# Kernel tuning notes

Measured on AMD Instinct MI355X. Metric: run time of the kernel, lower is better.

## Reference

```python
import jax, jax.numpy as jnp
import numpy as np
from jax import lax

V = 9; C1 = 80; C2 = 40; C4 = 24; CH = 32
H1, W1 = 30, 40; H2, W2 = 60, 80; H4, W4 = 120, 160
SHAPE = (96, 96, 96); N = 131072; EPS = 1e-5
OFFS = np.stack(np.meshgrid(np.arange(-1, 2), np.arange(-1, 2), np.arange(-1, 2), indexing='ij'), -1).reshape(-1, 3).astype(np.int32)  # 27 kernel offsets


def conv2d(x, w, b):
    y = lax.conv_general_dilated(x, w, (1, 1), 'SAME', dimension_numbers=('NCHW', 'OIHW', 'NCHW'))
    return y + b[None, :, None, None]


def bn1d(x, g, b):  # eval-mode BatchNorm1d (running_mean=0, running_var=1)
    return g * x * (1.0 / np.sqrt(1.0 + EPS)) + b


def layernorm(x, g, b):
    m = x.mean(-1, keepdims=True)
    v = ((x - m) ** 2).mean(-1, keepdims=True)
    return (x - m) / jnp.sqrt(v + EPS) * g + b


def grid_sample_zeros(img, gx, gy):
    # img [V,C,H,W]; gx,gy [V,M] normalized to [-1,1]; bilinear, align_corners=True, zeros padding
    Vn, C, H, W = img.shape
    px = (gx + 1.0) * 0.5 * (W - 1)
    py = (gy + 1.0) * 0.5 * (H - 1)
    x0 = jnp.floor(px); y0 = jnp.floor(py)
    wx = px - x0; wy = py - y0
    flat = img.reshape(Vn, C, H * W)
    def corner(xc, yc, wgt):
        valid = (xc >= 0) & (xc <= W - 1) & (yc >= 0) & (yc <= H - 1)
        xi = jnp.clip(xc, 0, W - 1).astype(jnp.int32)
        yi = jnp.clip(yc, 0, H - 1).astype(jnp.int32)
        idx = yi * W + xi  # [V,M]
        g = jax.vmap(lambda f, i: f[:, i])(flat, idx)  # [V,C,M]
        return g * (wgt * valid)[:, None, :]
    return (corner(x0, y0, (1 - wx) * (1 - wy)) + corner(x0 + 1, y0, wx * (1 - wy))
            + corner(x0, y0 + 1, (1 - wx) * wy) + corner(x0 + 1, y0 + 1, wx * wy))


def subm_conv(feat, W3, cxyz, grid):
    # submanifold sparse 3x3x3 conv: per-offset gather of active neighbors -> GEMM -> accumulate
    n = feat.shape[0]
    shp = jnp.asarray(SHAPE, jnp.int32)
    out = jnp.zeros((n, W3.shape[-1]), feat.dtype)
    for k in range(27):
        nc = cxyz + jnp.asarray(OFFS[k])
        inb = jnp.all((nc >= 0) & (nc < shp), axis=1)
        ncc = jnp.clip(nc, 0, shp - 1)
        idx = grid[ncc[:, 0], ncc[:, 1], ncc[:, 2]]
        ok = (inb & (idx >= 0)).astype(feat.dtype)
        g = feat[jnp.clip(idx, 0, n - 1)] * ok[:, None]
        out = out + g @ W3[k]
    return out


def _forward(feats_1x, feats_2x, feats_4x, origin, voxel_size, KRcam,
             w_f1, b_f1, w_f2, b_f2, w_f4, b_f4, w_down, b_down,
             w_p1, b_p1, w_p2, b_p2, w_p3, b_p3, w_p4, b_p4,
             bn0_g, bn0_b, w_elan, w_s1, ln1_g, ln1_b, w_s2, ln2_g, ln2_b,
             w_s3, ln3_g, ln3_b, w_s4, bn4_g, bn4_b,
             coords, stage, min_view_number):
    # feat_fusion_pre (bs=1, take batch 0)
    f1 = jax.nn.relu(conv2d(feats_1x[:, 0], w_f1, b_f1))
    f2 = jax.nn.relu(conv2d(feats_2x[:, 0], w_f2, b_f2))
    f4 = jax.nn.relu(conv2d(feats_4x[:, 0], w_f4, b_f4))
    f1 = jax.image.resize(f1, (V, C1, H2, W2), 'bilinear')  # F.interpolate x2
    f4 = f4.reshape(V, C4, H2, 2, W2, 2).mean(axis=(3, 5))  # AvgPool2d(2)
    fuse = jnp.concatenate([f1, f2, f4], axis=1)
    fuse = jax.nn.relu(conv2d(fuse, w_down, b_down))
    for w, b in ((w_p1, b_p1), (w_p2, b_p2), (w_p3, b_p3), (w_p4, b_p4)):
        fuse = fuse + jax.nn.relu(conv2d(fuse, w, b))  # residual blocks -> [V,CH,H2,W2]
    # multi-view projection
    cxyz = coords[:, 1:]
    world = cxyz.astype(jnp.float32) * voxel_size + origin[0]
    hom = jnp.concatenate([world, jnp.ones_like(world[:, :1])], axis=1)  # [N,4]
    im_p = jnp.einsum('vij,nj->vin', KRcam[:, 0], hom)  # [V,3,N]
    im_z = im_p[:, 2]
    gx = 2.0 * (im_p[:, 0] / im_z) / (W4 - 1) - 1.0
    gy = 2.0 * (im_p[:, 1] / im_z) / (H4 - 1) - 1.0
    mask = (jnp.abs(gx) <= 1) & (jnp.abs(gy) <= 1) & (im_z > 0)  # [V,N]
    count = mask.sum(0).astype(jnp.float32)
    # inputs are constructed so every voxel is seen by all views: valid_voxel compaction == identity
    feats = grid_sample_zeros(fuse, gx, gy) * mask[:, None, :]  # [V,CH,N]
    feat = feats.transpose(2, 0, 1)  # [N,V,CH]
    m = mask.T.astype(feat.dtype)  # [N,V]
    den = m.sum(1, keepdims=True)
    mean = (m[..., None] * feat).sum(1) / den
    var = (m[..., None] * (feat - mean[:, None, :]) ** 2).sum(1) / den  # [N,CH]
    # sparse subm conv chain
    sc = cxyz // (2 ** (2 - stage))  # stage=2 -> identity
    grid = jnp.full(SHAPE, -1, jnp.int32).at[sc[:, 0], sc[:, 1], sc[:, 2]].set(jnp.arange(N, dtype=jnp.int32))
    x = bn1d(var, bn0_g, bn0_b)
    x = jax.nn.relu(subm_conv(x, w_elan, sc, grid))  # Spares3dELAN stand-in
    r = jax.nn.relu(subm_conv(x, w_s1, sc, grid)); x = layernorm(r + x, ln1_g, ln1_b)
    r = jax.nn.relu(subm_conv(x, w_s2, sc, grid)); x = layernorm(r + x, ln2_g, ln2_b)
    r = jax.nn.relu(subm_conv(x, w_s3, sc, grid)); x = layernorm(r + x, ln3_g, ln3_b)
    occ = bn1d(subm_conv(x, w_s4, sc, grid), bn4_g, bn4_b)  # [N,1]
    return occ, coords, count


def setup_inputs() -> dict:
    key = jax.random.key(0)
    keys = jax.random.split(key, 40)
    ki = iter(range(40))
    def rn(shape, s=1.0):
        return jax.random.normal(keys[next(ki)], shape, jnp.float32) * s
    inp = {}
    inp['feats_1x'] = rn((V, 1, C1, H1, W1))
    inp['feats_2x'] = rn((V, 1, C2, H2, W2))
    inp['feats_4x'] = rn((V, 1, C4, H4, W4))
    flat = np.arange(N, dtype=np.int64) * 6  # unique active voxels in a 96^3 grid
    cx = flat // (96 * 96); rem = flat % (96 * 96)
    inp['coords'] = jnp.asarray(np.stack([np.zeros(N, np.int64), cx, rem // 96, rem % 96], 1), jnp.int32)
    inp['origin'] = jnp.asarray([[-1.92, -1.92, 1.0]], jnp.float32)
    inp['voxel_size'] = jnp.float32(0.04)
    fx, fy = 38.0, 28.0
    P = np.zeros((V, 1, 3, 4), np.float32)
    for v in range(V):
        P[v, 0] = np.array([[fx, 0.0, (W4 - 1) / 2, fx * 0.02 * (v - 4)],
                            [0.0, fy, (H4 - 1) / 2, 0.0],
                            [0.0, 0.0, 1.0, 0.0]], np.float32)
    inp['KRcam'] = jnp.asarray(P)
    s = 0.05
    inp['w_f1'] = rn((C1, C1, 3, 3), s); inp['b_f1'] = rn((C1,), s)
    inp['w_f2'] = rn((C2, C2, 3, 3), s); inp['b_f2'] = rn((C2,), s)
    inp['w_f4'] = rn((C4, C4, 3, 3), s); inp['b_f4'] = rn((C4,), s)
    inp['w_down'] = rn((CH, C1 + C2 + C4, 1, 1), s); inp['b_down'] = rn((CH,), s)
    for i in (1, 2, 3, 4):
        inp['w_p%d' % i] = rn((CH, CH, 3, 3), s); inp['b_p%d' % i] = rn((CH,), s)
    inp['bn0_g'] = jnp.ones((CH,), jnp.float32); inp['bn0_b'] = jnp.zeros((CH,), jnp.float32)
    inp['w_elan'] = rn((27, CH, CH), s)
    inp['w_s1'] = rn((27, CH, CH), s); inp['ln1_g'] = jnp.ones((CH,), jnp.float32); inp['ln1_b'] = jnp.zeros((CH,), jnp.float32)
    inp['w_s2'] = rn((27, CH, CH), s); inp['ln2_g'] = jnp.ones((CH,), jnp.float32); inp['ln2_b'] = jnp.zeros((CH,), jnp.float32)
    inp['w_s3'] = rn((27, CH, CH), s); inp['ln3_g'] = jnp.ones((CH,), jnp.float32); inp['ln3_b'] = jnp.zeros((CH,), jnp.float32)
    inp['w_s4'] = rn((27, CH, 1), s); inp['bn4_g'] = jnp.ones((1,), jnp.float32); inp['bn4_b'] = jnp.zeros((1,), jnp.float32)
    inp['stage'] = 2
    inp['min_view_number'] = 1
    return inp


def reference(feats_1x, feats_2x, feats_4x, origin, voxel_size, KRcam,
              w_f1, b_f1, w_f2, b_f2, w_f4, b_f4, w_down, b_down,
              w_p1, b_p1, w_p2, b_p2, w_p3, b_p3, w_p4, b_p4,
              bn0_g, bn0_b, w_elan, w_s1, ln1_g, ln1_b, w_s2, ln2_g, ln2_b,
              w_s3, ln3_g, ln3_b, w_s4, bn4_g, bn4_b,
              coords, stage, min_view_number):
    return _forward(feats_1x, feats_2x, feats_4x, origin, voxel_size, KRcam,
                    w_f1, b_f1, w_f2, b_f2, w_f4, b_f4, w_down, b_down,
                    w_p1, b_p1, w_p2, b_p2, w_p3, b_p3, w_p4, b_p4,
                    bn0_g, bn0_b, w_elan, w_s1, ln1_g, ln1_b, w_s2, ln2_g, ln2_b,
                    w_s3, ln3_g, ln3_b, w_s4, bn4_g, bn4_b,
                    coords, stage, min_view_number)
```

## Files before the change

kernel.cpp:

```cpp
#include <hip/hip_runtime.h>
#include <math.h>

#define VN 9
#define NVOX 131072
#define GS 96
static constexpr float INVS = 0.9999950000374997f;

typedef short bf16x8 __attribute__((ext_vector_type(8)));
typedef float f32x4v __attribute__((ext_vector_type(4)));

__device__ inline float4 ld4(const float* p){ return *reinterpret_cast<const float4*>(p); }

__device__ inline ushort f2b(float f){
  unsigned u = __float_as_uint(f);
  unsigned r = (u + 0x7fffu + ((u >> 16) & 1u)) >> 16;
  return (ushort)r;
}
__device__ inline float b2f(ushort s){ return __uint_as_float(((unsigned)s) << 16); }
__device__ inline float blo(unsigned u){ return __uint_as_float(u << 16); }
__device__ inline float bhi(unsigned u){ return __uint_as_float(u & 0xffff0000u); }

__device__ inline float4 ld4b(const ushort* p){
  uint2 u = *reinterpret_cast<const uint2*>(p);
  float4 r; r.x = blo(u.x); r.y = bhi(u.x); r.z = blo(u.y); r.w = bhi(u.y); return r;
}
__device__ inline void st4b(ushort* p, float4 v){
  uint2 u;
  u.x = (unsigned)f2b(v.x) | ((unsigned)f2b(v.y) << 16);
  u.y = (unsigned)f2b(v.z) | ((unsigned)f2b(v.w) << 16);
  *reinterpret_cast<uint2*>(p) = u;
}

__device__ inline void wprep2_dev(const float* __restrict__ w, ushort* __restrict__ o,
                                  int Cout, int Cin, int K, int CK, int CoutPad, int tid){
  int ci32 = tid & 31;
  int co = (tid >> 5) % CoutPad;
  int ck = (tid / (32*CoutPad)) % CK;
  int tap = tid / (32*CoutPad*CK);
  int ci = ck*32 + ci32;
  float v = 0.f;
  if (co < Cout && ci < Cin) v = w[(size_t)(co*Cin + ci)*K*K + tap];
  o[tid] = f2b(v);
}
__device__ inline void wprep_dev(const float* __restrict__ w, ushort* __restrict__ o, int tid){
  int k = tid >> 10;
  int r = tid & 1023;
  int co = r >> 5;
  int ci = r & 31;
  o[tid] = f2b(w[k*1024 + ci*32 + co]);
}

__device__ inline void nhwc_tile_dev(const float* __restrict__ in, ushort* __restrict__ out,
                                     int C, int Cpad, int HW, int tile, int tilesPerV,
                                     float* lds, int tx){
  int v  = tile / tilesPerV;
  int p0 = (tile - v*tilesPerV) * 64;
  const float* ip = in + (size_t)v*C*HW + p0;
  int iters = Cpad >> 2;
  for (int i = 0; i < iters; ++i){
    int idx = i*256 + tx;
    int c = idx >> 6;
    int p = idx & 63;
    float val = 0.f;
    if (c < C && (p0 + p) < HW) val = ip[(size_t)c*HW + p];
    lds[c*65 + p] = val;
  }
  __syncthreads();
  int groups = Cpad >> 2;
  int tot = 64*groups;
  for (int basei = 0; basei < tot; basei += 256){
    int idx = basei + tx;
    if (idx < tot){
      int g  = idx % groups;
      int px = idx / groups;
      if ((p0 + px) < HW){
        float4 r;
        r.x = lds[(g*4+0)*65 + px];
        r.y = lds[(g*4+1)*65 + px];
        r.z = lds[(g*4+2)*65 + px];
        r.w = lds[(g*4+3)*65 + px];
        st4b(out + (size_t)(v*HW + p0 + px)*Cpad + g*4, r);
      }
    }
  }
}

__global__ __launch_bounds__(256) void k_prep(
    const float* wf1s, const float* wf2s, const float* wf4s, const float* wdns,
    const float* wp0s, const float* wp1s, const float* wp2s, const float* wp3s,
    const float* wes, const float* ws1s, const float* ws2s, const float* ws3s,
    ushort* wf1, ushort* wf2, ushort* wf4, ushort* wdn,
    ushort* wp0, ushort* wp1, ushort* wp2, ushort* wp3,
    ushort* w2e, ushort* w2s1, ushort* w2s2, ushort* w2s3,
    int* grid,
    const float* f1, const float* f2, const float* f4,
    ushort* o1, ushort* o2, ushort* o4){
  __shared__ float lds[96*65];
  int bid = blockIdx.x;
  int tx = threadIdx.x;
  if (bid < 270){ int t = bid*256+tx; if (t < 69120) wprep2_dev(wf1s, wf1, 80, 80, 3, 3, 80, t); return; }
  bid -= 270;
  if (bid < 108){ int t = bid*256+tx; if (t < 27648) wprep2_dev(wf2s, wf2, 40, 40, 3, 2, 48, t); return; }
  bid -= 108;
  if (bid < 36){ int t = bid*256+tx; if (t < 9216) wprep2_dev(wf4s, wf4, 24, 24, 3, 1, 32, t); return; }
  bid -= 36;
  if (bid < 20){ int t = bid*256+tx; if (t < 5120) wprep2_dev(wdns, wdn, 32, 144, 1, 5, 32, t); return; }
  bid -= 20;
  if (bid < 36){ int t = bid*256+tx; if (t < 9216) wprep2_dev(wp0s, wp0, 32, 32, 3, 1, 32, t); return; }
  bid -= 36;
  if (bid < 36){ int t = bid*256+tx; if (t < 9216) wprep2_dev(wp1s, wp1, 32, 32, 3, 1, 32, t); return; }
  bid -= 36;
  if (bid < 36){ int t = bid*256+tx; if (t < 9216) wprep2_dev(wp2s, wp2, 32, 32, 3, 1, 32, t); return; }
  bid -= 36;
  if (bid < 36){ int t = bid*256+tx; if (t < 9216) wprep2_dev(wp3s, wp3, 32, 32, 3, 1, 32, t); return; }
  bid -= 36;
  if (bid < 108){ int t = bid*256+tx; if (t < 27648) wprep_dev(wes, w2e, t); return; }
  bid -= 108;
  if (bid < 108){ int t = bid*256+tx; if (t < 27648) wprep_dev(ws1s, w2s1, t); return; }
  bid -= 108;
  if (bid < 108){ int t = bid*256+tx; if (t < 27648) wprep_dev(ws2s, w2s2, t); return; }
  bid -= 108;
  if (bid < 108){ int t = bid*256+tx; if (t < 27648) wprep_dev(ws3s, w2s3, t); return; }
  bid -= 108;
  if (bid < 3456){ int t = bid*256+tx; if (t < GS*GS*GS) grid[t] = -1; return; }
  bid -= 3456;
  if (bid < 171){ nhwc_tile_dev(f1, o1, 80, 96, 1200, bid, 19, lds, tx); return; }
  bid -= 171;
  if (bid < 675){ nhwc_tile_dev(f2, o2, 40, 64, 4800, bid, 75, lds, tx); return; }
  bid -= 675;
  if (bid < 2700){ nhwc_tile_dev(f4, o4, 24, 32, 19200, bid, 300, lds, tx); }
}

template<int CK, int NT, int TAPS, int MT>
__global__ __launch_bounds__(256) void k_conv_mfma(
    const ushort* __restrict__ fin, const ushort* __restrict__ w2,
    const float* __restrict__ bias, ushort* __restrict__ outp,
    int H, int W, int total, int Cout, int outStride, int outOff,
    const ushort* __restrict__ skipin){
  constexpr int CIN = CK*32;
  constexpr int COP = NT*16;
  int lane = threadIdx.x & 63;
  int wave = threadIdx.x >> 6;
  int vbase = blockIdx.x*(MT*64) + wave*(MT*16);
  int m = lane & 15, q = lane >> 4;
  int HW = H*W;
  int p[MT], py[MT], px[MT]; bool pin[MT];
  #pragma unroll
  for (int t = 0; t < MT; ++t){
    int pp = vbase + t*16 + m;
    pin[t] = pp < total;
    if (pp > total-1) pp = total-1;
    p[t] = pp;
    int v = pp / HW; int rem = pp - v*HW;
    int y = rem / W;
    py[t] = y; px[t] = rem - y*W;
  }
  f32x4v acc[MT][NT];
  #pragma unroll
  for (int t = 0; t < MT; ++t)
    #pragma unroll
    for (int n = 0; n < NT; ++n) acc[t][n] = 0.f;
  bf16x8 z = (short)0;

  #pragma unroll 1
  for (int tap = 0; tap < TAPS; ++tap){
    int dy = (TAPS == 9) ? tap/3 - 1 : 0;
    int dx = (TAPS == 9) ? tap%3 - 1 : 0;
    int off = dy*W + dx;
    bool val[MT];
    #pragma unroll
    for (int t = 0; t < MT; ++t)
      val[t] = pin[t] && ((unsigned)(py[t]+dy) < (unsigned)H)
                      && ((unsigned)(px[t]+dx) < (unsigned)W);
    #pragma unroll
    for (int ck = 0; ck < CK; ++ck){
      bf16x8 Af[MT], Bf[NT];
      #pragma unroll
      for (int t = 0; t < MT; ++t){
        size_t idx = val[t] ? (size_t)(p[t]+off) : 0;
        bf16x8 a = *(const bf16x8*)(fin + idx*CIN + ck*32 + q*8);
        Af[t] = val[t] ? a : z;
      }
      #pragma unroll
      for (int n = 0; n < NT; ++n)
        Bf[n] = *(const bf16x8*)(w2 + ((size_t)((tap*CK+ck)*COP + n*16 + m))*32 + q*8);
      #pragma unroll
      for (int t = 0; t < MT; ++t)
        #pragma unroll
        for (int n = 0; n < NT; ++n)
          acc[t][n] = __builtin_amdgcn_mfma_f32_16x16x32_bf16(Af[t], Bf[n], acc[t][n], 0, 0, 0);
    }
  }

  #pragma unroll
  for (int n = 0; n < NT; ++n){
    int co = n*16 + m;
    bool cok = co < Cout;
    float bs = cok ? bias[co] : 0.f;
    #pragma unroll
    for (int t = 0; t < MT; ++t){
      #pragma unroll
      for (int r = 0; r < 4; ++r){
        int pp = vbase + t*16 + q*4 + r;
        if (pp < total && cok){
          float x = fmaxf(acc[t][n][r] + bs, 0.f);
          if (skipin) x += b2f(skipin[(size_t)pp*CIN + co]);
          outp[(size_t)pp*outStride + outOff + co] = f2b(x);
        }
      }
    }
  }
}

__global__ void k_respool(const ushort* __restrict__ t1, const ushort* __restrict__ t4,
                          ushort* __restrict__ fc){
  int tid = blockIdx.x*256 + threadIdx.x;
  if (tid < 864000){
    int c4 = tid % 20;
    int x  = (tid / 20) % 80;
    int y  = (tid / 1600) % 60;
    int v  = tid / 96000;
    int c = c4*4;
    int ky = y >> 1; int y0, y1; float wy0, wy1;
    if ((y & 1) == 0){ y0 = ky-1; y1 = ky; wy0 = 0.25f; wy1 = 0.75f; if (y0 < 0){ y0 = 0; wy0 = 0.f; wy1 = 1.f; } }
    else             { y0 = ky; y1 = ky+1; wy0 = 0.75f; wy1 = 0.25f; if (y1 > 29){ y1 = 29; wy1 = 0.f; wy0 = 1.f; } }
    int kx = x >> 1; int x0, x1; float wx0, wx1;
    if ((x & 1) == 0){ x0 = kx-1; x1 = kx; wx0 = 0.25f; wx1 = 0.75f; if (x0 < 0){ x0 = 0; wx0 = 0.f; wx1 = 1.f; } }
    else             { x0 = kx; x1 = kx+1; wx0 = 0.75f; wx1 = 0.25f; if (x1 > 39){ x1 = 39; wx1 = 0.f; wx0 = 1.f; } }
    float4 a00 = ld4b(t1 + ((size_t)(v*30 + y0)*40 + x0)*80 + c);
    float4 a01 = ld4b(t1 + ((size_t)(v*30 + y0)*40 + x1)*80 + c);
    float4 a10 = ld4b(t1 + ((size_t)(v*30 + y1)*40 + x0)*80 + c);
    float4 a11 = ld4b(t1 + ((size_t)(v*30 + y1)*40 + x1)*80 + c);
    float w00 = wy0*wx0, w01 = wy0*wx1, w10 = wy1*wx0, w11 = wy1*wx1;
    float4 r;
    r.x = w00*a00.x + w01*a01.x + w10*a10.x + w11*a11.x;
    r.y = w00*a00.y + w01*a01.y + w10*a10.y + w11*a11.y;
    r.z = w00*a00.z + w01*a01.z + w10*a10.z + w11*a11.z;
    r.w = w00*a00.w + w01*a01.w + w10*a10.w + w11*a11.w;
    st4b(fc + ((size_t)(v*60 + y)*80 + x)*160 + c, r);
    return;
  }
  int t = tid - 864000;
  if (t >= 432000) return;
  int c4 = t % 10;
  int x  = (t / 10) % 80;
  int y  = (t / 800) % 60;
  int v  = t / 48000;
  if (c4 < 6){
    int c = c4*4;
    const ushort* b0 = t4 + ((size_t)(v*120 + 2*y)*160 + 2*x)*24 + c;
    float4 a = ld4b(b0), b = ld4b(b0 + 24), cc = ld4b(b0 + 160*24), d = ld4b(b0 + 160*24 + 24);
    float4 r;
    r.x = 0.25f*(a.x + b.x + cc.x + d.x);
    r.y = 0.25f*(a.y + b.y + cc.y + d.y);
    r.z = 0.25f*(a.z + b.z + cc.z + d.z);
    r.w = 0.25f*(a.w + b.w + cc.w + d.w);
    st4b(fc + ((size_t)(v*60 + y)*80 + x)*160 + 120 + c, r);
  } else {
    float4 zz = {0.f,0.f,0.f,0.f};
    st4b(fc + ((size_t)(v*60 + y)*80 + x)*160 + 144 + (c4-6)*4, zz);
  }
}

__global__ void k_scatter(const int* __restrict__ coords, const int* __restrict__ stage,
                          int* __restrict__ grid, int* __restrict__ scn,
                          float* __restrict__ coords_out,
                          const float* __restrict__ origin, const float* __restrict__ vsz,
                          const float* __restrict__ KR,
                          uint4* __restrict__ samp, float* __restrict__ cnt){
  int n = blockIdx.x*256 + threadIdx.x;
  if (n >= NVOX) return;
  int c0 = coords[n*4], c1 = coords[n*4+1], c2 = coords[n*4+2], c3 = coords[n*4+3];
  coords_out[n*4+0] = (float)c0;
  coords_out[n*4+1] = (float)c1;
  coords_out[n*4+2] = (float)c2;
  coords_out[n*4+3] = (float)c3;
  int sh = 2 - stage[0];
  int s1 = c1 >> sh, s2 = c2 >> sh, s3 = c3 >> sh;
  scn[n*3+0] = s1; scn[n*3+1] = s2; scn[n*3+2] = s3;
  grid[(s1*GS + s2)*GS + s3] = n;

  float vs = vsz[0];
  float wx = (float)c1*vs + origin[0];
  float wy = (float)c2*vs + origin[1];
  float wz = (float)c3*vs + origin[2];
  float den = 0.f;
  #pragma unroll 1
  for (int v = 0; v < VN; ++v){
    const float* P = KR + v*12;
    float ix = P[0]*wx + P[1]*wy + P[2]*wz + P[3];
    float iy = P[4]*wx + P[5]*wy + P[6]*wz + P[7];
    float iz = P[8]*wx + P[9]*wy + P[10]*wz + P[11];
    float rz = 1.f/iz;
    float gx = 2.f*(ix*rz)/159.f - 1.f;
    float gy = 2.f*(iy*rz)/119.f - 1.f;
    bool ok = (fabsf(gx) <= 1.f) && (fabsf(gy) <= 1.f) && (iz > 0.f);
    float px = ok ? (gx + 1.f)*0.5f*79.f : 0.f;
    float py = ok ? (gy + 1.f)*0.5f*59.f : 0.f;
    float x0f = floorf(px), y0f = floorf(py);
    float fx = px - x0f, fy = py - y0f;
    int idx = (int)y0f*80 + (int)x0f;
    float mf = ok ? 1.f : 0.f;
    float w00 = (1.f-fx)*(1.f-fy)*mf, w01 = fx*(1.f-fy)*mf;
    float w10 = (1.f-fx)*fy*mf,       w11 = fx*fy*mf;
    uint4 s;
    s.x = (unsigned)idx;
    s.y = (unsigned)f2b(w00) | ((unsigned)f2b(w01) << 16);
    s.z = (unsigned)f2b(w10) | ((unsigned)f2b(w11) << 16);
    s.w = 0;
    samp[(size_t)v*NVOX + n] = s;
    den += mf;
  }
  cnt[n] = den;
}

__global__ __launch_bounds__(256) void k_nbr_sample(
    const int* __restrict__ scn, const int* __restrict__ grid,
    int* __restrict__ nbr, unsigned* __restrict__ gmask16,
    const ushort* __restrict__ fuse, const uint4* __restrict__ samp,
    const float* __restrict__ cnt, const float* __restrict__ bn0g,
    const float* __restrict__ bn0b, ushort* __restrict__ F0){
  if (blockIdx.x < 512){
    int n = blockIdx.x*256 + threadIdx.x;
    int lane = threadIdx.x & 63;
    int sx = scn[n*3+0], sy = scn[n*3+1], sz = scn[n*3+2];
    unsigned msk = 0;
    #pragma unroll 1
    for (int k = 0; k < 27; ++k){
      int dx = k/9 - 1, dy = (k/3)%3 - 1, dz = k%3 - 1;
      int nx = sx+dx, ny = sy+dy, nz = sz+dz;
      int idx = -1;
      if (((unsigned)nx < 96u) && ((unsigned)ny < 96u) && ((unsigned)nz < 96u))
        idx = grid[(nx*GS + ny)*GS + nz];
      nbr[k*NVOX + n] = idx;
      unsigned long long b = __ballot(idx >= 0);
      unsigned sub = (unsigned)((b >> ((lane >> 4)*16)) & 0xFFFFull);
      if (sub) msk |= (1u << k);
    }
    if ((lane & 15) == 0) gmask16[n >> 4] = msk;
    return;
  }
  int tid = (blockIdx.x - 512)*256 + threadIdx.x;
  int vox = tid >> 3;
  int c4 = tid & 7;
  int c = c4*4;
  float s0=0.f,s1=0.f,s2=0.f,s3=0.f;
  float q0=0.f,q1=0.f,q2=0.f,q3=0.f;
  #pragma unroll 1
  for (int v = 0; v < VN; ++v){
    uint4 sv = samp[(size_t)v*NVOX + vox];
    float w00 = blo(sv.y), w01 = bhi(sv.y);
    float w10 = blo(sv.z), w11 = bhi(sv.z);
    const ushort* bp = fuse + (size_t)v*153600 + (size_t)sv.x*32 + c;
    float4 a00 = ld4b(bp);
    float4 a01 = ld4b(bp + 32);
    float4 a10 = ld4b(bp + 2560);
    float4 a11 = ld4b(bp + 2592);
    float g0 = w00*a00.x + w01*a01.x + w10*a10.x + w11*a11.x;
    float g1 = w00*a00.y + w01*a01.y + w10*a10.y + w11*a11.y;
    float g2 = w00*a00.z + w01*a01.z + w10*a10.z + w11*a11.z;
    float g3 = w00*a00.w + w01*a01.w + w10*a10.w + w11*a11.w;
    s0 += g0; q0 += g0*g0;
    s1 += g1; q1 += g1*g1;
    s2 += g2; q2 += g2*g2;
    s3 += g3; q3 += g3*g3;
  }
  float iden = 1.f/cnt[vox];
  float m0 = s0*iden, m1 = s1*iden, m2 = s2*iden, m3 = s3*iden;
  float4 g = ld4(bn0g + c);
  float4 b = ld4(bn0b + c);
  float4 r;
  r.x = g.x*fmaxf(q0*iden - m0*m0, 0.f)*INVS + b.x;
  r.y = g.y*fmaxf(q1*iden - m1*m1, 0.f)*INVS + b.y;
  r.z = g.z*fmaxf(q2*iden - m2*m2, 0.f)*INVS + b.z;
  r.w = g.w*fmaxf(q3*iden - m3*m3, 0.f)*INVS + b.w;
  st4b(F0 + (size_t)vox*32 + c, r);
}

template<int MODE>
__global__ __launch_bounds__(256, 8) void k_subm_mfma(
    const ushort* __restrict__ fin, const ushort* __restrict__ w2,
    const int* __restrict__ nbr, const unsigned* __restrict__ gmask16,
    const float* __restrict__ lng, const float* __restrict__ lnb,
    ushort* __restrict__ fout){
  int lane = threadIdx.x & 63;
  int wave = threadIdx.x >> 6;
  int vb = blockIdx.x*64 + wave*16;
  int m = lane & 15;
  int q = lane >> 4;

  f32x4v acc0 = 0.f, acc1 = 0.f;
  bf16x8 zc = (short)0;
  unsigned rem = gmask16[vb >> 4];
  int id = -1;
  int k = -1;
  if (rem){
    k = __ffs(rem) - 1; rem &= rem - 1;
    id = nbr[(size_t)k*NVOX + vb + m];
  }
  while (k >= 0){
    bf16x8 A;
    {
      bf16x8 a = *(const bf16x8*)(fin + (size_t)(id < 0 ? 0 : id)*32 + q*8);
      A = (id < 0) ? zc : a;
    }
    bf16x8 b0 = *(const bf16x8*)(w2 + (size_t)(k*32 + m)*32 + q*8);
    bf16x8 b1 = *(const bf16x8*)(w2 + (size_t)(k*32 + 16 + m)*32 + q*8);
    int k2 = -1, id2 = -1;
    if (rem){
      k2 = __ffs(rem) - 1; rem &= rem - 1;
      id2 = nbr[(size_t)k2*NVOX + vb + m];
    }
    acc0 = __builtin_amdgcn_mfma_f32_16x16x32_bf16(A, b0, acc0, 0, 0, 0);
    acc1 = __builtin_amdgcn_mfma_f32_16x16x32_bf16(A, b1, acc1, 0, 0, 0);
    id = id2; k = k2;
  }

  int ch0 = m, ch1 = 16 + m;
  float g0 = 0.f, g1 = 0.f, bb0 = 0.f, bb1 = 0.f;
  if (MODE == 1){ g0 = lng[ch0]; g1 = lng[ch1]; bb0 = lnb[ch0]; bb1 = lnb[ch1]; }
  #pragma unroll
  for (int r = 0; r < 4; ++r){
    int vox = vb + q*4 + r;
    float x0 = fmaxf(acc0[r], 0.f);
    float x1 = fmaxf(acc1[r], 0.f);
    if (MODE == 1){
      x0 += b2f(fin[(size_t)vox*32 + ch0]);
      x1 += b2f(fin[(size_t)vox*32 + ch1]);
      float s = x0 + x1;
      s += __shfl_xor(s, 1, 16);
      s += __shfl_xor(s, 2, 16);
      s += __shfl_xor(s, 4, 16);
      s += __shfl_xor(s, 8, 16);
      float mean = s * (1.f/32.f);
      float d0 = x0 - mean, d1 = x1 - mean;
      float v2 = d0*d0 + d1*d1;
      v2 += __shfl_xor(v2, 1, 16);
      v2 += __shfl_xor(v2, 2, 16);
      v2 += __shfl_xor(v2, 4, 16);
      v2 += __shfl_xor(v2, 8, 16);
      float rs = 1.f / sqrtf(v2*(1.f/32.f) + 1e-5f);
      x0 = d0*rs*g0 + bb0;
      x1 = d1*rs*g1 + bb1;
    }
    fout[(size_t)vox*32 + ch0] = f2b(x0);
    fout[(size_t)vox*32 + ch1] = f2b(x1);
  }
}

__global__ __launch_bounds__(256) void k_s4(
    const ushort* __restrict__ fin, const float* __restrict__ w4,
    const int* __restrict__ nbr, const unsigned* __restrict__ gmask16,
    const float* __restrict__ bn4g, const float* __restrict__ bn4b,
    float* __restrict__ occ){
  int n = blockIdx.x*256 + threadIdx.x;
  if (n >= NVOX) return;
  unsigned gm = gmask16[n >> 4];
  float acc = 0.f;
  #pragma unroll 1
  for (int k = 0; k < 27; ++k){
    if (!((gm >> k) & 1u)) continue;
    int idx = nbr[(size_t)k*NVOX + n];
    if (idx >= 0){
      const uint4* r4 = (const uint4*)(fin + (size_t)idx*32);
      const float* wk = w4 + k*32;
      #pragma unroll
      for (int u = 0; u < 4; ++u){
        uint4 d = r4[u];
        const float* w8 = wk + u*8;
        acc += blo(d.x)*w8[0] + bhi(d.x)*w8[1];
        acc += blo(d.y)*w8[2] + bhi(d.y)*w8[3];
        acc += blo(d.z)*w8[4] + bhi(d.z)*w8[5];
        acc += blo(d.w)*w8[6] + bhi(d.w)*w8[7];
      }
    }
  }
  occ[n] = bn4g[0]*acc*INVS + bn4b[0];
}

extern "C" void kernel_launch(void* const* d_in, const int* in_sizes, int n_in,
                              void* d_out, int out_size, void* d_ws, size_t ws_size,
                              hipStream_t stream){
  const float* feats1 = (const float*)d_in[0];
  const float* feats2 = (const float*)d_in[1];
  const float* feats4 = (const float*)d_in[2];
  const int*   coords = (const int*)d_in[3];
  const float* origin = (const float*)d_in[4];
  const float* vsz    = (const float*)d_in[5];
  const float* KR     = (const float*)d_in[6];
  const float* w_f1 = (const float*)d_in[7];  const float* b_f1 = (const float*)d_in[8];
  const float* w_f2 = (const float*)d_in[9];  const float* b_f2 = (const float*)d_in[10];
  const float* w_f4 = (const float*)d_in[11]; const float* b_f4 = (const float*)d_in[12];
  const float* w_dn = (const float*)d_in[13]; const float* b_dn = (const float*)d_in[14];
  const float* w_p[4] = {(const float*)d_in[15], (const float*)d_in[17],
                         (const float*)d_in[19], (const float*)d_in[21]};
  const float* b_p[4] = {(const float*)d_in[16], (const float*)d_in[18],
                         (const float*)d_in[20], (const float*)d_in[22]};
  const float* bn0g = (const float*)d_in[23]; const float* bn0b = (const float*)d_in[24];
  const float* w_elan = (const float*)d_in[25];
  const float* w_s1 = (const float*)d_in[26]; const float* ln1g = (const float*)d_in[27]; const float* ln1b = (const float*)d_in[28];
  const float* w_s2 = (const float*)d_in[29]; const float* ln2g = (const float*)d_in[30]; const float* ln2b = (const float*)d_in[31];
  const float* w_s3 = (const float*)d_in[32]; const float* ln3g = (const float*)d_in[33]; const float* ln3b = (const float*)d_in[34];
  const float* w_s4 = (const float*)d_in[35]; const float* bn4g = (const float*)d_in[36]; const float* bn4b = (const float*)d_in[37];
  const int* stage  = (const int*)d_in[38];
  float* out = (float*)d_out;
  char* base = (char*)d_ws;

  size_t off = 0;
  auto alloc = [&](size_t bytes)->char*{ char* p = base + off; off += (bytes + 255) & ~(size_t)255; return p; };
  ushort* nhwc1 = (ushort*)alloc((size_t)9*30*40*96*2);
  ushort* nhwc2 = (ushort*)alloc((size_t)9*60*80*64*2);
  ushort* nhwc4 = (ushort*)alloc((size_t)9*120*160*32*2);
  ushort* t1    = (ushort*)alloc((size_t)9*30*40*80*2);
  ushort* t4    = (ushort*)alloc((size_t)9*120*160*24*2);
  ushort* fcat  = (ushort*)alloc((size_t)9*60*80*160*2);
  ushort* A     = (ushort*)alloc((size_t)9*60*80*32*2);
  ushort* B     = (ushort*)alloc((size_t)9*60*80*32*2);
  ushort* Fb0   = (ushort*)alloc((size_t)NVOX*32*2);
  ushort* Fb1   = (ushort*)alloc((size_t)NVOX*32*2);
  int*    nbr   = (int*)alloc((size_t)27*NVOX*4);
  int*    grid  = (int*)alloc((size_t)GS*GS*GS*4);
  int*    scn   = (int*)alloc((size_t)NVOX*3*4);
  unsigned* gmask16 = (unsigned*)alloc((size_t)(NVOX/16)*4);
  ushort* wf1   = (ushort*)alloc(9*3*80*32*2);
  ushort* wf2   = (ushort*)alloc(9*2*48*32*2);
  ushort* wf4   = (ushort*)alloc(9*1*32*32*2);
  ushort* wdn   = (ushort*)alloc(1*5*32*32*2);
  ushort* wp0   = (ushort*)alloc(9*1*32*32*2);
  ushort* wp1   = (ushort*)alloc(9*1*32*32*2);
  ushort* wp2   = (ushort*)alloc(9*1*32*32*2);
  ushort* wp3   = (ushort*)alloc(9*1*32*32*2);
  ushort* w2e   = (ushort*)alloc(27*1024*2);
  ushort* w2s1  = (ushort*)alloc(27*1024*2);
  ushort* w2s2  = (ushort*)alloc(27*1024*2);
  ushort* w2s3  = (ushort*)alloc(27*1024*2);
  uint4* samp = (uint4*)nhwc2;

  auto nb = [](int total){ return (total + 255)/256; };

  k_prep<<<8012,256,0,stream>>>(
      w_f1, w_f2, w_f4, w_dn, w_p[0], w_p[1], w_p[2], w_p[3],
      w_elan, w_s1, w_s2, w_s3,
      wf1, wf2, wf4, wdn, wp0, wp1, wp2, wp3, w2e, w2s1, w2s2, w2s3, grid,
      feats1, feats2, feats4, nhwc1, nhwc2, nhwc4);

  k_conv_mfma<3,5,9,1><<<169,256,0,stream>>>(nhwc1, wf1, b_f1, t1, 30, 40, 10800, 80, 80, 0, nullptr);
  k_conv_mfma<2,3,9,1><<<675,256,0,stream>>>(nhwc2, wf2, b_f2, fcat, 60, 80, 43200, 40, 160, 80, nullptr);
  k_conv_mfma<1,2,9,4><<<675,256,0,stream>>>(nhwc4, wf4, b_f4, t4, 120, 160, 172800, 24, 24, 0, nullptr);

  k_respool<<<nb(864000 + 432000),256,0,stream>>>(t1, t4, fcat);

  k_conv_mfma<5,2,1,1><<<675,256,0,stream>>>(fcat, wdn, b_dn, A, 60, 80, 43200, 32, 32, 0, nullptr);
  k_conv_mfma<1,2,9,1><<<675,256,0,stream>>>(A, wp0, b_p[0], B, 60, 80, 43200, 32, 32, 0, A);
  k_conv_mfma<1,2,9,1><<<675,256,0,stream>>>(B, wp1, b_p[1], A, 60, 80, 43200, 32, 32, 0, B);
  k_conv_mfma<1,2,9,1><<<675,256,0,stream>>>(A, wp2, b_p[2], B, 60, 80, 43200, 32, 32, 0, A);
  k_conv_mfma<1,2,9,1><<<675,256,0,stream>>>(B, wp3, b_p[3], A, 60, 80, 43200, 32, 32, 0, B);

  k_scatter<<<nb(NVOX),256,0,stream>>>(coords, stage, grid, scn, out + NVOX,
                                       origin, vsz, KR, samp, out + 5*NVOX);

  k_nbr_sample<<<512 + NVOX/32,256,0,stream>>>(scn, grid, nbr, gmask16,
                                               A, samp, out + 5*NVOX, bn0g, bn0b, Fb0);

  k_subm_mfma<0><<<NVOX/64,256,0,stream>>>(Fb0, w2e,  nbr, gmask16, nullptr, nullptr, Fb1);
  k_subm_mfma<1><<<NVOX/64,256,0,stream>>>(Fb1, w2s1, nbr, gmask16, ln1g, ln1b, Fb0);
  k_subm_mfma<1><<<NVOX/64,256,0,stream>>>(Fb0, w2s2, nbr, gmask16, ln2g, ln2b, Fb1);
  k_subm_mfma<1><<<NVOX/64,256,0,stream>>>(Fb1, w2s3, nbr, gmask16, ln3g, ln3b, Fb0);
  k_s4<<<nb(NVOX),256,0,stream>>>(Fb0, w_s4, nbr, gmask16, bn4g, bn4b, out);
}
```

Baseline: 389.7 us.

## Merge head convs with scatter, fuse respool with neighbor build, deepen gather prefetch

The three image-head convolutions and the voxel scatter now run in one launch, split by block index. Resample/pool and neighbor-table construction are merged into a second launch, and the neighbor build is spread across four waves per 64 voxels, combining masks with shared-memory atomics. The sampling kernel prefetches the next view's sample record, and the sparse conv and final head loops prefetch neighbor rows two steps ahead. The aim is fewer launches, more independent blocks in flight, and hidden gather latency. The cost is more register pressure and a new sample buffer placed at an offset not visible here.

```diff
diff --git a/kernel.cpp b/kernel.cpp
--- a/kernel.cpp
+++ b/kernel.cpp
@@ -132,16 +132,16 @@
 }
 
 template<int CK, int NT, int TAPS, int MT>
-__global__ __launch_bounds__(256) void k_conv_mfma(
+__device__ void conv_dev(
     const ushort* __restrict__ fin, const ushort* __restrict__ w2,
     const float* __restrict__ bias, ushort* __restrict__ outp,
     int H, int W, int total, int Cout, int outStride, int outOff,
-    const ushort* __restrict__ skipin){
+    const ushort* __restrict__ skipin, int bid, int tid){
   constexpr int CIN = CK*32;
   constexpr int COP = NT*16;
-  int lane = threadIdx.x & 63;
-  int wave = threadIdx.x >> 6;
-  int vbase = blockIdx.x*(MT*64) + wave*(MT*16);
+  int lane = tid & 63;
+  int wave = tid >> 6;
+  int vbase = bid*(MT*64) + wave*(MT*16);
   int m = lane & 15, q = lane >> 4;
   int HW = H*W;
   int p[MT], py[MT], px[MT]; bool pin[MT];
@@ -212,64 +212,22 @@
   }
 }
 
-__global__ void k_respool(const ushort* __restrict__ t1, const ushort* __restrict__ t4,
-                          ushort* __restrict__ fc){
-  int tid = blockIdx.x*256 + threadIdx.x;
-  if (tid < 864000){
-    int c4 = tid % 20;
-    int x  = (tid / 20) % 80;
-    int y  = (tid / 1600) % 60;
-    int v  = tid / 96000;
-    int c = c4*4;
-    int ky = y >> 1; int y0, y1; float wy0, wy1;
-    if ((y & 1) == 0){ y0 = ky-1; y1 = ky; wy0 = 0.25f; wy1 = 0.75f; if (y0 < 0){ y0 = 0; wy0 = 0.f; wy1 = 1.f; } }
-    else             { y0 = ky; y1 = ky+1; wy0 = 0.75f; wy1 = 0.25f; if (y1 > 29){ y1 = 29; wy1 = 0.f; wy0 = 1.f; } }
-    int kx = x >> 1; int x0, x1; float wx0, wx1;
-    if ((x & 1) == 0){ x0 = kx-1; x1 = kx; wx0 = 0.25f; wx1 = 0.75f; if (x0 < 0){ x0 = 0; wx0 = 0.f; wx1 = 1.f; } }
-    else             { x0 = kx; x1 = kx+1; wx0 = 0.75f; wx1 = 0.25f; if (x1 > 39){ x1 = 39; wx1 = 0.f; wx0 = 1.f; } }
-    float4 a00 = ld4b(t1 + ((size_t)(v*30 + y0)*40 + x0)*80 + c);
-    float4 a01 = ld4b(t1 + ((size_t)(v*30 + y0)*40 + x1)*80 + c);
-    float4 a10 = ld4b(t1 + ((size_t)(v*30 + y1)*40 + x0)*80 + c);
-    float4 a11 = ld4b(t1 + ((size_t)(v*30 + y1)*40 + x1)*80 + c);
-    float w00 = wy0*wx0, w01 = wy0*wx1, w10 = wy1*wx0, w11 = wy1*wx1;
-    float4 r;
-    r.x = w00*a00.x + w01*a01.x + w10*a10.x + w11*a11.x;
-    r.y = w00*a00.y + w01*a01.y + w10*a10.y + w11*a11.y;
-    r.z = w00*a00.z + w01*a01.z + w10*a10.z + w11*a11.z;
-    r.w = w00*a00.w + w01*a01.w + w10*a10.w + w11*a11.w;
-    st4b(fc + ((size_t)(v*60 + y)*80 + x)*160 + c, r);
-    return;
-  }
-  int t = tid - 864000;
-  if (t >= 432000) return;
-  int c4 = t % 10;
-  int x  = (t / 10) % 80;
-  int y  = (t / 800) % 60;
-  int v  = t / 48000;
-  if (c4 < 6){
-    int c = c4*4;
-    const ushort* b0 = t4 + ((size_t)(v*120 + 2*y)*160 + 2*x)*24 + c;
-    float4 a = ld4b(b0), b = ld4b(b0 + 24), cc = ld4b(b0 + 160*24), d = ld4b(b0 + 160*24 + 24);
-    float4 r;
-    r.x = 0.25f*(a.x + b.x + cc.x + d.x);
-    r.y = 0.25f*(a.y + b.y + cc.y + d.y);
-    r.z = 0.25f*(a.z + b.z + cc.z + d.z);
-    r.w = 0.25f*(a.w + b.w + cc.w + d.w);
-    st4b(fc + ((size_t)(v*60 + y)*80 + x)*160 + 120 + c, r);
-  } else {
-    float4 zz = {0.f,0.f,0.f,0.f};
-    st4b(fc + ((size_t)(v*60 + y)*80 + x)*160 + 144 + (c4-6)*4, zz);
-  }
-}
-
-__global__ void k_scatter(const int* __restrict__ coords, const int* __restrict__ stage,
-                          int* __restrict__ grid, int* __restrict__ scn,
-                          float* __restrict__ coords_out,
-                          const float* __restrict__ origin, const float* __restrict__ vsz,
-                          const float* __restrict__ KR,
-                          uint4* __restrict__ samp, float* __restrict__ cnt){
-  int n = blockIdx.x*256 + threadIdx.x;
-  if (n >= NVOX) return;
+template<int CK, int NT, int TAPS, int MT>
+__global__ __launch_bounds__(256) void k_conv_mfma(
+    const ushort* __restrict__ fin, const ushort* __restrict__ w2,
+    const float* __restrict__ bias, ushort* __restrict__ outp,
+    int H, int W, int total, int Cout, int outStride, int outOff,
+    const ushort* __restrict__ skipin){
+  conv_dev<CK,NT,TAPS,MT>(fin, w2, bias, outp, H, W, total, Cout, outStride, outOff,
+                          skipin, blockIdx.x, threadIdx.x);
+}
+
+__device__ void scatter_dev(const int* __restrict__ coords, const int* __restrict__ stage,
+                            int* __restrict__ grid, int* __restrict__ scn,
+                            float* __restrict__ coords_out,
+                            const float* __restrict__ origin, const float* __restrict__ vsz,
+                            const float* __restrict__ KR,
+                            uint4* __restrict__ samp, float* __restrict__ cnt, int n){
   int c0 = coords[n*4], c1 = coords[n*4+1], c2 = coords[n*4+2], c3 = coords[n*4+3];
   coords_out[n*4+0] = (float)c0;
   coords_out[n*4+1] = (float)c1;
@@ -314,41 +272,123 @@
   cnt[n] = den;
 }
 
-__global__ __launch_bounds__(256) void k_nbr_sample(
+__global__ __launch_bounds__(256) void k_heads(
+    const ushort* nhwc1, const ushort* wf1, const float* b_f1, ushort* t1,
+    const ushort* nhwc2, const ushort* wf2, const float* b_f2, ushort* fcat,
+    const ushort* nhwc4, const ushort* wf4, const float* b_f4, ushort* t4,
+    const int* coords, const int* stage, int* grid, int* scn, float* coords_out,
+    const float* origin, const float* vsz, const float* KR, uint4* samp, float* cnt){
+  int bid = blockIdx.x;
+  int tid = threadIdx.x;
+  if (bid < 169){ conv_dev<3,5,9,1>(nhwc1, wf1, b_f1, t1, 30, 40, 10800, 80, 80, 0, nullptr, bid, tid); return; }
+  bid -= 169;
+  if (bid < 675){ conv_dev<2,3,9,1>(nhwc2, wf2, b_f2, fcat, 60, 80, 43200, 40, 160, 80, nullptr, bid, tid); return; }
+  bid -= 675;
+  if (bid < 675){ conv_dev<1,2,9,4>(nhwc4, wf4, b_f4, t4, 120, 160, 172800, 24, 24, 0, nullptr, bid, tid); return; }
+  bid -= 675;
+  { int n = bid*256 + tid;
+    scatter_dev(coords, stage, grid, scn, coords_out, origin, vsz, KR, samp, cnt, n); }
+}
+
+__global__ __launch_bounds__(256) void k_respool_nbr(
+    const ushort* __restrict__ t1, const ushort* __restrict__ t4, ushort* __restrict__ fc,
     const int* __restrict__ scn, const int* __restrict__ grid,
-    int* __restrict__ nbr, unsigned* __restrict__ gmask16,
+    int* __restrict__ nbr, unsigned* __restrict__ gmask16){
+  __shared__ unsigned m16[4];
+  int bid = blockIdx.x;
+  int tidx = threadIdx.x;
+  if (bid < 5063){
+    int tid = bid*256 + tidx;
+    if (tid < 864000){
+      int c4 = tid % 20;
+      int x  = (tid / 20) % 80;
+      int y  = (tid / 1600) % 60;
+      int v  = tid / 96000;
+      int c = c4*4;
+      int ky = y >> 1; int y0, y1; float wy0, wy1;
+      if ((y & 1) == 0){ y0 = ky-1; y1 = ky; wy0 = 0.25f; wy1 = 0.75f; if (y0 < 0){ y0 = 0; wy0 = 0.f; wy1 = 1.f; } }
+      else             { y0 = ky; y1 = ky+1; wy0 = 0.75f; wy1 = 0.25f; if (y1 > 29){ y1 = 29; wy1 = 0.f; wy0 = 1.f; } }
+      int kx = x >> 1; int x0, x1; float wx0, wx1;
+      if ((x & 1) == 0){ x0 = kx-1; x1 = kx; wx0 = 0.25f; wx1 = 0.75f; if (x0 < 0){ x0 = 0; wx0 = 0.f; wx1 = 1.f; } }
+      else             { x0 = kx; x1 = kx+1; wx0 = 0.75f; wx1 = 0.25f; if (x1 > 39){ x1 = 39; wx1 = 0.f; wx0 = 1.f; } }
+      float4 a00 = ld4b(t1 + ((size_t)(v*30 + y0)*40 + x0)*80 + c);
+      float4 a01 = ld4b(t1 + ((size_t)(v*30 + y0)*40 + x1)*80 + c);
+      float4 a10 = ld4b(t1 + ((size_t)(v*30 + y1)*40 + x0)*80 + c);
+      float4 a11 = ld4b(t1 + ((size_t)(v*30 + y1)*40 + x1)*80 + c);
+      float w00 = wy0*wx0, w01 = wy0*wx1, w10 = wy1*wx0, w11 = wy1*wx1;
+      float4 r;
+      r.x = w00*a00.x + w01*a01.x + w10*a10.x + w11*a11.x;
+      r.y = w00*a00.y + w01*a01.y + w10*a10.y + w11*a11.y;
+      r.z = w00*a00.z + w01*a01.z + w10*a10.z + w11*a11.z;
+      r.w = w00*a00.w + w01*a01.w + w10*a10.w + w11*a11.w;
+      st4b(fc + ((size_t)(v*60 + y)*80 + x)*160 + c, r);
+      return;
+    }
+    int t = tid - 864000;
+    if (t >= 432000) return;
+    int c4 = t % 10;
+    int x  = (t / 10) % 80;
+    int y  = (t / 800) % 60;
+    int v  = t / 48000;
+    if (c4 < 6){
+      int c = c4*4;
+      const ushort* b0 = t4 + ((size_t)(v*120 + 2*y)*160 + 2*x)*24 + c;
+      float4 a = ld4b(b0), b = ld4b(b0 + 24), cc = ld4b(b0 + 160*24), d = ld4b(b0 + 160*24 + 24);
+      float4 r;
+      r.x = 0.25f*(a.x + b.x + cc.x + d.x);
+      r.y = 0.25f*(a.y + b.y + cc.y + d.y);
+      r.z = 0.25f*(a.z + b.z + cc.z + d.z);
+      r.w = 0.25f*(a.w + b.w + cc.w + d.w);
+      st4b(fc + ((size_t)(v*60 + y)*80 + x)*160 + 120 + c, r);
+    } else {
+      float4 zz = {0.f,0.f,0.f,0.f};
+      st4b(fc + ((size_t)(v*60 + y)*80 + x)*160 + 144 + (c4-6)*4, zz);
+    }
+    return;
+  }
+  bid -= 5063;
+  if (tidx < 4) m16[tidx] = 0;
+  __syncthreads();
+  int vb = bid*64;
+  int lane = tidx & 63;
+  int wv = tidx >> 6;
+  int n = vb + lane;
+  int sx = scn[n*3+0], sy = scn[n*3+1], sz = scn[n*3+2];
+  int k0 = wv*7;
+  int k1 = min(27, k0 + 7);
+  unsigned msk = 0;
+  #pragma unroll 1
+  for (int k = k0; k < k1; ++k){
+    int dx = k/9 - 1, dy = (k/3)%3 - 1, dz = k%3 - 1;
+    int nx = sx+dx, ny = sy+dy, nz = sz+dz;
+    int idx = -1;
+    if (((unsigned)nx < 96u) && ((unsigned)ny < 96u) && ((unsigned)nz < 96u))
+      idx = grid[(nx*GS + ny)*GS + nz];
+    nbr[(size_t)k*NVOX + n] = idx;
+    unsigned long long b = __ballot(idx >= 0);
+    unsigned sub = (unsigned)((b >> ((lane >> 4)*16)) & 0xFFFFull);
+    if (sub) msk |= (1u << k);
+  }
+  if ((lane & 15) == 0 && msk) atomicOr(&m16[lane >> 4], msk);
+  __syncthreads();
+  if (tidx < 4) gmask16[(vb >> 4) + tidx] = m16[tidx];
+}
+
+__global__ __launch_bounds__(256) void k_sample(
     const ushort* __restrict__ fuse, const uint4* __restrict__ samp,
     const float* __restrict__ cnt, const float* __restrict__ bn0g,
     const float* __restrict__ bn0b, ushort* __restrict__ F0){
-  if (blockIdx.x < 512){
-    int n = blockIdx.x*256 + threadIdx.x;
-    int lane = threadIdx.x & 63;
-    int sx = scn[n*3+0], sy = scn[n*3+1], sz = scn[n*3+2];
-    unsigned msk = 0;
-    #pragma unroll 1
-    for (int k = 0; k < 27; ++k){
-      int dx = k/9 - 1, dy = (k/3)%3 - 1, dz = k%3 - 1;
-      int nx = sx+dx, ny = sy+dy, nz = sz+dz;
-      int idx = -1;
-      if (((unsigned)nx < 96u) && ((unsigned)ny < 96u) && ((unsigned)nz < 96u))
-        idx = grid[(nx*GS + ny)*GS + nz];
-      nbr[k*NVOX + n] = idx;
-      unsigned long long b = __ballot(idx >= 0);
-      unsigned sub = (unsigned)((b >> ((lane >> 4)*16)) & 0xFFFFull);
-      if (sub) msk |= (1u << k);
-    }
-    if ((lane & 15) == 0) gmask16[n >> 4] = msk;
-    return;
-  }
-  int tid = (blockIdx.x - 512)*256 + threadIdx.x;
+  int tid = blockIdx.x*256 + threadIdx.x;
   int vox = tid >> 3;
   int c4 = tid & 7;
   int c = c4*4;
   float s0=0.f,s1=0.f,s2=0.f,s3=0.f;
   float q0=0.f,q1=0.f,q2=0.f,q3=0.f;
+  uint4 sv = samp[vox];
   #pragma unroll 1
   for (int v = 0; v < VN; ++v){
-    uint4 sv = samp[(size_t)v*NVOX + vox];
+    uint4 svn = sv;
+    if (v+1 < VN) svn = samp[(size_t)(v+1)*NVOX + vox];
     float w00 = blo(sv.y), w01 = bhi(sv.y);
     float w10 = blo(sv.z), w11 = bhi(sv.z);
     const ushort* bp = fuse + (size_t)v*153600 + (size_t)sv.x*32 + c;
@@ -364,6 +404,7 @@
     s1 += g1; q1 += g1*g1;
     s2 += g2; q2 += g2*g2;
     s3 += g3; q3 += g3*g3;
+    sv = svn;
   }
   float iden = 1.f/cnt[vox];
   float m0 = s0*iden, m1 = s1*iden, m2 = s2*iden, m3 = s3*iden;
@@ -392,28 +433,28 @@
   f32x4v acc0 = 0.f, acc1 = 0.f;
   bf16x8 zc = (short)0;
   unsigned rem = gmask16[vb >> 4];
-  int id = -1;
-  int k = -1;
-  if (rem){
-    k = __ffs(rem) - 1; rem &= rem - 1;
-    id = nbr[(size_t)k*NVOX + vb + m];
-  }
-  while (k >= 0){
-    bf16x8 A;
-    {
-      bf16x8 a = *(const bf16x8*)(fin + (size_t)(id < 0 ? 0 : id)*32 + q*8);
-      A = (id < 0) ? zc : a;
-    }
-    bf16x8 b0 = *(const bf16x8*)(w2 + (size_t)(k*32 + m)*32 + q*8);
-    bf16x8 b1 = *(const bf16x8*)(w2 + (size_t)(k*32 + 16 + m)*32 + q*8);
+  int k0 = -1, k1 = -1;
+  int id0 = -1, id1 = -1;
+  if (rem){ k0 = __ffs(rem) - 1; rem &= rem - 1; id0 = nbr[(size_t)k0*NVOX + vb + m]; }
+  if (rem){ k1 = __ffs(rem) - 1; rem &= rem - 1; id1 = nbr[(size_t)k1*NVOX + vb + m]; }
+  bf16x8 A0 = zc;
+  if (k0 >= 0){
+    bf16x8 a = *(const bf16x8*)(fin + (size_t)(id0 < 0 ? 0 : id0)*32 + q*8);
+    A0 = (id0 < 0) ? zc : a;
+  }
+  while (k0 >= 0){
+    bf16x8 A1 = zc;
+    if (k1 >= 0){
+      bf16x8 a = *(const bf16x8*)(fin + (size_t)(id1 < 0 ? 0 : id1)*32 + q*8);
+      A1 = (id1 < 0) ? zc : a;
+    }
     int k2 = -1, id2 = -1;
-    if (rem){
-      k2 = __ffs(rem) - 1; rem &= rem - 1;
-      id2 = nbr[(size_t)k2*NVOX + vb + m];
-    }
-    acc0 = __builtin_amdgcn_mfma_f32_16x16x32_bf16(A, b0, acc0, 0, 0, 0);
-    acc1 = __builtin_amdgcn_mfma_f32_16x16x32_bf16(A, b1, acc1, 0, 0, 0);
-    id = id2; k = k2;
+    if (rem){ k2 = __ffs(rem) - 1; rem &= rem - 1; id2 = nbr[(size_t)k2*NVOX + vb + m]; }
+    bf16x8 b0 = *(const bf16x8*)(w2 + (size_t)(k0*32 + m)*32 + q*8);
+    bf16x8 b1 = *(const bf16x8*)(w2 + (size_t)(k0*32 + 16 + m)*32 + q*8);
+    acc0 = __builtin_amdgcn_mfma_f32_16x16x32_bf16(A0, b0, acc0, 0, 0, 0);
+    acc1 = __builtin_amdgcn_mfma_f32_16x16x32_bf16(A0, b1, acc1, 0, 0, 0);
+    A0 = A1; id1 = id2; k0 = k1; k1 = k2;
   }
 
   int ch0 = m, ch1 = 16 + m;
@@ -455,12 +496,13 @@
     float* __restrict__ occ){
   int n = blockIdx.x*256 + threadIdx.x;
   if (n >= NVOX) return;
-  unsigned gm = gmask16[n >> 4];
+  unsigned rem = gmask16[n >> 4];
   float acc = 0.f;
-  #pragma unroll 1
-  for (int k = 0; k < 27; ++k){
-    if (!((gm >> k) & 1u)) continue;
-    int idx = nbr[(size_t)k*NVOX + n];
+  int k = -1, idx = -1;
+  if (rem){ k = __ffs(rem) - 1; rem &= rem - 1; idx = nbr[(size_t)k*NVOX + n]; }
+  while (k >= 0){
+    int k2 = -1, idx2 = -1;
+    if (rem){ k2 = __ffs(rem) - 1; rem &= rem - 1; idx2 = nbr[(size_t)k2*NVOX + n]; }
     if (idx >= 0){
       const uint4* r4 = (const uint4*)(fin + (size_t)idx*32);
       const float* wk = w4 + k*32;
@@ -474,6 +516,7 @@
         acc += blo(d.w)*w8[6] + bhi(d.w)*w8[7];
       }
     }
+    k = k2; idx = idx2;
   }
   occ[n] = bn4g[0]*acc*INVS + bn4b[0];
 }
@@ -544,11 +587,16 @@
       wf1, wf2, wf4, wdn, wp0, wp1, wp2, wp3, w2e, w2s1, w2s2, w2s3, grid,
       feats1, feats2, feats4, nhwc1, nhwc2, nhwc4);
 
-  k_conv_mfma<3,5,9,1><<<169,256,0,stream>>>(nhwc1, wf1, b_f1, t1, 30, 40, 10800, 80, 80, 0, nullptr);
-  k_conv_mfma<2,3,9,1><<<675,256,0,stream>>>(nhwc2, wf2, b_f2, fcat, 60, 80, 43200, 40, 160, 80, nullptr);
-  k_conv_mfma<1,2,9,4><<<675,256,0,stream>>>(nhwc4, wf4, b_f4, t4, 120, 160, 172800, 24, 24, 0, nullptr);
-
-  k_respool<<<nb(864000 + 432000),256,0,stream>>>(t1, t4, fcat);
+  k_heads<<<2031,256,0,stream>>>(
+      nhwc1, wf1, b_f1, t1,
+      nhwc2, wf2, b_f2, fcat,
+      nhwc4, wf4, b_f4, t4,
+      coords, stage, grid, scn, out + NVOX,
+      origin, vsz, KR, (uint4*)(base + off), out + 5*NVOX);
+  uint4* samp2 = (uint4*)(base + off);
+  (void)samp;
+
+  k_respool_nbr<<<5063 + 2048,256,0,stream>>>(t1, t4, fcat, scn, grid, nbr, gmask16);
 
   k_conv_mfma<5,2,1,1><<<675,256,0,stream>>>(fcat, wdn, b_dn, A, 60, 80, 43200, 32, 32, 0, nullptr);
   k_conv_mfma<1,2,9,1><<<675,256,0,stream>>>(A, wp0, b_p[0], B, 60, 80, 43200, 32, 32, 0, A);
@@ -556,15 +604,12 @@
   k_conv_mfma<1,2,9,1><<<675,256,0,stream>>>(A, wp2, b_p[2], B, 60, 80, 43200, 32, 32, 0, A);
   k_conv_mfma<1,2,9,1><<<675,256,0,stream>>>(B, wp3, b_p[3], A, 60, 80, 43200, 32, 32, 0, B);
 
-  k_scatter<<<nb(NVOX),256,0,stream>>>(coords, stage, grid, scn, out + NVOX,
-                                       origin, vsz, KR, samp, out + 5*NVOX);
-
-  k_nbr_sample<<<512 + NVOX/32,256,0,stream>>>(scn, grid, nbr, gmask16,
-                                               A, samp, out + 5*NVOX, bn0g, bn0b, Fb0);
+  k_sample<<<NVOX/32,256,0,stream>>>(A, samp2, out + 5*NVOX, bn0g, bn0b, Fb0);
 
   k_subm_mfma<0><<<NVOX/64,256,0,stream>>>(Fb0, w2e,  nbr, gmask16, nullptr, nullptr, Fb1);
   k_subm_mfma<1><<<NVOX/64,256,0,stream>>>(Fb1, w2s1, nbr, gmask16, ln1g, ln1b, Fb0);
   k_subm_mfma<1><<<NVOX/64,256,0,stream>>>(Fb0, w2s2, nbr, gmask16, ln2g, ln2b, Fb1);
   k_subm_mfma<1><<<NVOX/64,256,0,stream>>>(Fb1, w2s3, nbr, gmask16, ln3g, ln3b, Fb0);
+
   k_s4<<<nb(NVOX),256,0,stream>>>(Fb0, w_s4, nbr, gmask16, bn4g, bn4b, out);
 }
```

Result: faster. 366.6 us (-5.9%).
